# Kernel optimization log

Measured on AMD Instinct MI355X. Metric: run time of the kernel, lower is better.

## Reference

```python
import jax, jax.numpy as jnp
import numpy as np

B, S, IN, H, NH, PF, L = 8, 1024, 256, 1024, 16, 4096, 6
HD = H // NH
EPS = 1e-5


def _layernorm(x, g, b):
    m = jnp.mean(x, axis=-1, keepdims=True)
    v = jnp.mean((x - m) ** 2, axis=-1, keepdims=True)
    return (x - m) * jax.lax.rsqrt(v + EPS) * g + b


def setup_inputs() -> dict:
    key = jax.random.key(0)
    ks = iter(jax.random.split(key, 40))
    sd = 0.02
    inp = {
        "input_x": jax.random.normal(next(ks), (B, S, IN), jnp.float32),
        "emb_W": jax.random.normal(next(ks), (IN, H), jnp.float32) * sd,
        "emb_b": jnp.zeros((H,), jnp.float32),
        "pos_tab": jax.random.normal(next(ks), (S, H), jnp.float32) * sd,
        "Wq": jax.random.normal(next(ks), (L, H, H), jnp.float32) * sd,
        "bq": jnp.zeros((L, H), jnp.float32),
        "Wk": jax.random.normal(next(ks), (L, H, H), jnp.float32) * sd,
        "bk": jnp.zeros((L, H), jnp.float32),
        "Wv": jax.random.normal(next(ks), (L, H, H), jnp.float32) * sd,
        "bv": jnp.zeros((L, H), jnp.float32),
        "Wo": jax.random.normal(next(ks), (L, H, H), jnp.float32) * sd,
        "bo": jnp.zeros((L, H), jnp.float32),
        "ln1_g": jnp.ones((L, H), jnp.float32),
        "ln1_b": jnp.zeros((L, H), jnp.float32),
        "W1": jax.random.normal(next(ks), (L, H, PF), jnp.float32) * sd,
        "b1": jnp.zeros((L, PF), jnp.float32),
        "W2": jax.random.normal(next(ks), (L, PF, H), jnp.float32) * sd,
        "b2": jnp.zeros((L, H), jnp.float32),
        "ln2_g": jnp.ones((L, H), jnp.float32),
        "ln2_b": jnp.zeros((L, H), jnp.float32),
    }
    return inp


def _encoder(input_x, emb_W, emb_b, pos_tab, Wq, bq, Wk, bk, Wv, bv, Wo, bo,
             ln1_g, ln1_b, W1, b1, W2, b2, ln2_g, ln2_b):
    scale = jnp.sqrt(jnp.float32(H))  # module scales by sqrt(hidden_size)
    x = (input_x @ emb_W + emb_b) * scale + pos_tab[None, :, :]  # [B,S,H]

    def layer(x, p):
        wq, bq_, wk, bk_, wv, bv_, wo, bo_, g1, be1, w1, b1_, w2, b2_, g2, be2 = p
        q = (x @ wq + bq_).reshape(B, S, NH, HD).transpose(0, 2, 1, 3)  # bhsd
        k = (x @ wk + bk_).reshape(B, S, NH, HD).transpose(0, 2, 1, 3)
        v = (x @ wv + bv_).reshape(B, S, NH, HD).transpose(0, 2, 1, 3)
        energy = jnp.einsum("bhqd,bhkd->bhqk", q, k) / scale  # NOTE: /sqrt(H)
        attn = jax.nn.softmax(energy, axis=-1)
        o = jnp.einsum("bhqk,bhkd->bhqd", attn, v)
        o = o.transpose(0, 2, 1, 3).reshape(B, S, H) @ wo + bo_
        x = _layernorm(x + o, g1, be1)
        f = jax.nn.relu(x @ w1 + b1_) @ w2 + b2_
        x = _layernorm(x + f, g2, be2)
        return x, None

    params = (Wq, bq, Wk, bk, Wv, bv, Wo, bo, ln1_g, ln1_b, W1, b1, W2, b2, ln2_g, ln2_b)
    x, _ = jax.lax.scan(layer, x, params)
    return x


def reference(input_x, emb_W, emb_b, pos_tab, Wq, bq, Wk, bk, Wv, bv, Wo, bo,
              ln1_g, ln1_b, W1, b1, W2, b2, ln2_g, ln2_b):
    return _encoder(input_x, emb_W, emb_b, pos_tab, Wq, bq, Wk, bk, Wv, bv,
                    Wo, bo, ln1_g, ln1_b, W1, b1, W2, b2, ln2_g, ln2_b)
```

## Files before the change

kernel.cpp:

```cpp
#include <hip/hip_runtime.h>

#define HDIM 1024
#define BB 8
#define SS 1024
#define NHEAD 16
#define PFF 4096
#define NLAYER 6
#define MM (BB*SS)

typedef __attribute__((ext_vector_type(8))) short bf16x8_t;
typedef __attribute__((ext_vector_type(4))) float f32x4_t;
typedef __attribute__((ext_vector_type(16))) float f32x16_t;

static __device__ __forceinline__ unsigned short f2b(float f) {
  unsigned int u = __float_as_uint(f);
  u += 0x7fffu + ((u >> 16) & 1u);
  return (unsigned short)(u >> 16);
}

static __device__ __forceinline__ unsigned pkbf(float lo, float hi) {
  unsigned r;
  asm("v_cvt_pk_bf16_f32 %0, %1, %2" : "=v"(r) : "v"(lo), "v"(hi));
  return r;
}

static __device__ __forceinline__ bf16x8_t mk8(unsigned a, unsigned b, unsigned c, unsigned d) {
  union { unsigned u[4]; bf16x8_t v; } x;
  x.u[0] = a; x.u[1] = b; x.u[2] = c; x.u[3] = d;
  return x.v;
}

static __device__ __forceinline__ void gload16(const void* g, void* l) {
  __builtin_amdgcn_global_load_lds((__attribute__((address_space(1))) void*)g,
                                   (__attribute__((address_space(3))) void*)l, 16, 0, 0);
}

__global__ __launch_bounds__(256) void cvt_bf16(const float* __restrict__ in,
                                                unsigned short* __restrict__ o, int n4) {
  const int i = blockIdx.x * 256 + threadIdx.x;
  if (i < n4) {
    const float4 v = ((const float4*)in)[i];
    ushort4 ob = { f2b(v.x), f2b(v.y), f2b(v.z), f2b(v.w) };
    ((ushort4*)o)[i] = ob;
  }
}

__global__ __launch_bounds__(256) void transpose_bf16(const float* __restrict__ in,
                                                      unsigned short* __restrict__ outT,
                                                      int R, int C) {
  __shared__ float tile[32][33];
  const int c0 = blockIdx.x * 32, r0 = blockIdx.y * 32;
  const int tx = threadIdx.x, ty = threadIdx.y;
#pragma unroll
  for (int i = 0; i < 4; ++i)
    tile[ty + 8*i][tx] = in[(size_t)(r0 + ty + 8*i) * C + c0 + tx];
  __syncthreads();
#pragma unroll
  for (int i = 0; i < 4; ++i)
    outT[(size_t)(c0 + ty + 8*i) * R + r0 + tx] = f2b(tile[tx][ty + 8*i]);
}

__global__ __launch_bounds__(256) void vtrans(const unsigned short* __restrict__ qkv,
                                              unsigned short* __restrict__ vt) {
  __shared__ unsigned short tile[32][34];
  const int s0 = blockIdx.x * 32;
  const int by = blockIdx.y;
  const int bh = by >> 1, dt = by & 1;
  const int b = bh >> 4, h = bh & 15;
  const int tx = threadIdx.x, ty = threadIdx.y;
  const unsigned short* src = qkv + ((size_t)(b * 1024 + s0)) * 3072 + 2048 + h * 64 + dt * 32;
#pragma unroll
  for (int i = 0; i < 4; ++i)
    tile[ty + 8*i][tx] = src[(size_t)(ty + 8*i) * 3072 + tx];
  __syncthreads();
  unsigned short* dst = vt + (size_t)(bh * 64 + dt * 32) * 1024 + s0;
#pragma unroll
  for (int i = 0; i < 4; ++i)
    dst[(size_t)(ty + 8*i) * 1024 + tx] = tile[tx][ty + 8*i];
}

__global__ __launch_bounds__(256) void concat_bias(const float* __restrict__ bq,
                                                   const float* __restrict__ bk,
                                                   const float* __restrict__ bv,
                                                   float* __restrict__ o) {
  const int i = blockIdx.x * 256 + threadIdx.x;
  o[i] = (i < 1024) ? bq[i] : ((i < 2048) ? bk[i - 1024] : bv[i - 2048]);
}

template<bool BIAS, bool RELU, bool RESID, bool EMB, bool WF32, bool WBF16>
__global__ __launch_bounds__(256) void gemm_bt(
    const unsigned short* __restrict__ A,
    const unsigned short* __restrict__ Bt,
    const float* __restrict__ bias,
    const float* __restrict__ resid,
    const float* __restrict__ pos,
    float* __restrict__ outf,
    unsigned short* __restrict__ outb,
    int M, int N, int K) {
  __shared__ __align__(1024) char smem[32768];
  const int t = threadIdx.x;
  const int lane = t & 63;
  const int w = t >> 6;
  const int wr = w >> 1, wc = w & 1;
  const int m0 = blockIdx.y * 128;
  const int n0 = blockIdx.x * 128;

  const f32x4_t z = {0.f, 0.f, 0.f, 0.f};
  f32x4_t acc[4][4];
#pragma unroll
  for (int i = 0; i < 4; ++i)
#pragma unroll
    for (int j = 0; j < 4; ++j) acc[i][j] = z;

  const int nkt = K >> 6;
  for (int kt = 0; kt < nkt; ++kt) {
#pragma unroll
    for (int i = 0; i < 4; ++i) {
      const int chunk = i * 4 + w;
      const int byteoff = chunk * 1024 + lane * 16;
      const int row = byteoff >> 7;
      const int scb = (byteoff & 127) ^ ((row & 7) << 4);
      gload16((const char*)A  + ((size_t)(m0 + row) * K + (kt << 6)) * 2 + scb,
              smem + chunk * 1024);
      gload16((const char*)Bt + ((size_t)(n0 + row) * K + (kt << 6)) * 2 + scb,
              smem + 16384 + chunk * 1024);
    }
    __syncthreads();
#pragma unroll
    for (int ks = 0; ks < 2; ++ks) {
      bf16x8_t af[4], bfv[4];
      const int cb = ks * 64 + ((lane >> 4) << 4);
#pragma unroll
      for (int i = 0; i < 4; ++i) {
        const int ra = wr * 64 + i * 16 + (lane & 15);
        af[i]  = *(const bf16x8_t*)(smem + ra * 128 + (cb ^ ((ra & 7) << 4)));
        const int rb = wc * 64 + i * 16 + (lane & 15);
        bfv[i] = *(const bf16x8_t*)(smem + 16384 + rb * 128 + (cb ^ ((rb & 7) << 4)));
      }
#pragma unroll
      for (int i = 0; i < 4; ++i)
#pragma unroll
        for (int j = 0; j < 4; ++j)
          acc[i][j] = __builtin_amdgcn_mfma_f32_16x16x32_bf16(af[i], bfv[j], acc[i][j], 0, 0, 0);
    }
    __syncthreads();
  }

#pragma unroll
  for (int i = 0; i < 4; ++i) {
    const int rbase = m0 + wr * 64 + i * 16 + ((lane >> 4) << 2);
#pragma unroll
    for (int j = 0; j < 4; ++j) {
      const int cc = n0 + wc * 64 + j * 16 + (lane & 15);
      float bv = 0.f;
      if (BIAS) bv = bias[cc];
#pragma unroll
      for (int r = 0; r < 4; ++r) {
        const int row = rbase + r;
        float v = acc[i][j][r] + bv;
        if (EMB)  v = v * 32.f + pos[(size_t)(row & (SS - 1)) * N + cc];
        if (RELU) v = fmaxf(v, 0.f);
        if (RESID) v += resid[(size_t)row * N + cc];
        if (WF32)  outf[(size_t)row * N + cc] = v;
        if (WBF16) outb[(size_t)row * N + cc] = f2b(v);
      }
    }
  }
}

__global__ __launch_bounds__(256) void attn2(
    const unsigned short* __restrict__ qkv,
    const unsigned short* __restrict__ vt,
    unsigned short* __restrict__ O) {
  __shared__ __align__(1024) char smem[2 * 16384];
  const int t = threadIdx.x, lane = t & 63, w = t >> 6;
  const int l31 = lane & 31, lg = lane >> 5;
  const int bh = blockIdx.y;
  const int b = bh >> 4, h = bh & 15;
  const size_t rowb = (size_t)b << 10;
  const int q0 = blockIdx.x * 128 + w * 32;

  bf16x8_t qf[4];
  {
    const unsigned short* Qp = qkv + (rowb + q0 + l31) * 3072 + h * 64 + lg * 8;
#pragma unroll
    for (int dd = 0; dd < 4; ++dd) qf[dd] = *(const bf16x8_t*)(Qp + dd * 16);
  }

  f32x16_t oa0, oa1;
#pragma unroll
  for (int r = 0; r < 16; ++r) { oa0[r] = 0.f; oa1[r] = 0.f; }
  float m_run = -1e30f, l_run = 0.f;
  const float inv32 = 1.f / 32.f;

  const char* kglob = (const char*)qkv + ((size_t)1024 + h * 64) * 2;
  const char* vglob = (const char*)vt + (size_t)bh * 64 * 1024 * 2;

  auto stage = [&](int kt, int buf) {
    char* kbuf = smem + buf * 16384;
    char* vbuf = kbuf + 8192;
#pragma unroll
    for (int i = 0; i < 2; ++i) {
      const int chunk = w * 2 + i;
      const int byteoff = chunk * 1024 + lane * 16;
      const int row = byteoff >> 7;
      const int scb = (byteoff & 127) ^ ((row & 7) << 4);
      gload16(kglob + (size_t)(rowb + kt * 64 + row) * 6144 + scb, kbuf + chunk * 1024);
      gload16(vglob + ((size_t)row * 1024 + kt * 64) * 2 + scb,    vbuf + chunk * 1024);
    }
  };

  stage(0, 0);
  for (int kt = 0; kt < 16; ++kt) {
    const int cb = kt & 1;
    __syncthreads();
    if (kt < 15) stage(kt + 1, cb ^ 1);
    const char* kbuf = smem + cb * 16384;
    const char* vbuf = kbuf + 8192;

    f32x16_t p0, p1;
#pragma unroll
    for (int r = 0; r < 16; ++r) { p0[r] = 0.f; p1[r] = 0.f; }
    __builtin_amdgcn_s_setprio(1);
#pragma unroll
    for (int dd = 0; dd < 4; ++dd) {
      {
        const int row = l31;
        const int col = (dd * 32 + (lg << 4)) ^ ((row & 7) << 4);
        bf16x8_t kf = *(const bf16x8_t*)(kbuf + row * 128 + col);
        p0 = __builtin_amdgcn_mfma_f32_32x32x16_bf16(kf, qf[dd], p0, 0, 0, 0);
      }
      {
        const int row = 32 + l31;
        const int col = (dd * 32 + (lg << 4)) ^ ((row & 7) << 4);
        bf16x8_t kf = *(const bf16x8_t*)(kbuf + row * 128 + col);
        p1 = __builtin_amdgcn_mfma_f32_32x32x16_bf16(kf, qf[dd], p1, 0, 0, 0);
      }
    }
    __builtin_amdgcn_s_setprio(0);

    float mx = p0[0];
#pragma unroll
    for (int r = 1; r < 16; ++r) mx = fmaxf(mx, p0[r]);
#pragma unroll
    for (int r = 0; r < 16; ++r) mx = fmaxf(mx, p1[r]);
    mx = fmaxf(mx, __shfl_xor(mx, 32));
    const float mn = fmaxf(m_run, mx * inv32);
    const float fr = __expf(m_run - mn);
    m_run = mn;
    float sum = 0.f;
#pragma unroll
    for (int r = 0; r < 16; ++r) { const float e = __expf(p0[r] * inv32 - mn); p0[r] = e; sum += e; }
#pragma unroll
    for (int r = 0; r < 16; ++r) { const float e = __expf(p1[r] * inv32 - mn); p1[r] = e; sum += e; }
    sum += __shfl_xor(sum, 32);
    l_run = l_run * fr + sum;
#pragma unroll
    for (int r = 0; r < 16; ++r) { oa0[r] *= fr; oa1[r] *= fr; }

    const unsigned A0 = pkbf(p0[0], p0[1]),  B0 = pkbf(p0[2], p0[3]);
    const unsigned C0 = pkbf(p0[4], p0[5]),  D0 = pkbf(p0[6], p0[7]);
    const unsigned E0 = pkbf(p0[8], p0[9]),  F0 = pkbf(p0[10], p0[11]);
    const unsigned G0 = pkbf(p0[12], p0[13]), H0 = pkbf(p0[14], p0[15]);
    const unsigned A1 = pkbf(p1[0], p1[1]),  B1 = pkbf(p1[2], p1[3]);
    const unsigned C1 = pkbf(p1[4], p1[5]),  D1 = pkbf(p1[6], p1[7]);
    const unsigned E1 = pkbf(p1[8], p1[9]),  F1 = pkbf(p1[10], p1[11]);
    const unsigned G1 = pkbf(p1[12], p1[13]), H1 = pkbf(p1[14], p1[15]);
    const unsigned sA0 = __shfl_xor((int)A0, 32), sB0 = __shfl_xor((int)B0, 32);
    const unsigned sC0 = __shfl_xor((int)C0, 32), sD0 = __shfl_xor((int)D0, 32);
    const unsigned sE0 = __shfl_xor((int)E0, 32), sF0 = __shfl_xor((int)F0, 32);
    const unsigned sG0 = __shfl_xor((int)G0, 32), sH0 = __shfl_xor((int)H0, 32);
    const unsigned sA1 = __shfl_xor((int)A1, 32), sB1 = __shfl_xor((int)B1, 32);
    const unsigned sC1 = __shfl_xor((int)C1, 32), sD1 = __shfl_xor((int)D1, 32);
    const unsigned sE1 = __shfl_xor((int)E1, 32), sF1 = __shfl_xor((int)F1, 32);
    const unsigned sG1 = __shfl_xor((int)G1, 32), sH1 = __shfl_xor((int)H1, 32);
    const bool hi = (lg != 0);
    bf16x8_t pf[4];
    pf[0] = hi ? mk8(sC0, sD0, C0, D0) : mk8(A0, B0, sA0, sB0);
    pf[1] = hi ? mk8(sG0, sH0, G0, H0) : mk8(E0, F0, sE0, sF0);
    pf[2] = hi ? mk8(sC1, sD1, C1, D1) : mk8(A1, B1, sA1, sB1);
    pf[3] = hi ? mk8(sG1, sH1, G1, H1) : mk8(E1, F1, sE1, sF1);

    __builtin_amdgcn_s_setprio(1);
#pragma unroll
    for (int c = 0; c < 4; ++c) {
      {
        const int row = l31;
        const int col = (c * 32 + (lg << 4)) ^ ((row & 7) << 4);
        bf16x8_t vf = *(const bf16x8_t*)(vbuf + row * 128 + col);
        oa0 = __builtin_amdgcn_mfma_f32_32x32x16_bf16(vf, pf[c], oa0, 0, 0, 0);
      }
      {
        const int row = 32 + l31;
        const int col = (c * 32 + (lg << 4)) ^ ((row & 7) << 4);
        bf16x8_t vf = *(const bf16x8_t*)(vbuf + row * 128 + col);
        oa1 = __builtin_amdgcn_mfma_f32_32x32x16_bf16(vf, pf[c], oa1, 0, 0, 0);
      }
    }
    __builtin_amdgcn_s_setprio(0);
  }

  const float inv = 1.f / l_run;
  unsigned short* op = O + (rowb + q0 + l31) * 1024 + h * 64 + (lg << 2);
#pragma unroll
  for (int rg = 0; rg < 4; ++rg) {
    const unsigned u0 = pkbf(oa0[rg * 4 + 0] * inv, oa0[rg * 4 + 1] * inv);
    const unsigned u1 = pkbf(oa0[rg * 4 + 2] * inv, oa0[rg * 4 + 3] * inv);
    uint2 st = { u0, u1 };
    *(uint2*)(op + rg * 8) = st;
    const unsigned v0 = pkbf(oa1[rg * 4 + 0] * inv, oa1[rg * 4 + 1] * inv);
    const unsigned v1 = pkbf(oa1[rg * 4 + 2] * inv, oa1[rg * 4 + 3] * inv);
    uint2 st2 = { v0, v1 };
    *(uint2*)(op + 32 + rg * 8) = st2;
  }
}

__global__ __launch_bounds__(256) void ln_kernel(
    const float* __restrict__ y, const float* __restrict__ g, const float* __restrict__ be,
    float* __restrict__ xf, unsigned short* __restrict__ xb) {
  const int row = blockIdx.x;
  const int t = threadIdx.x;
  const float4 v = ((const float4*)(y + (size_t)row * HDIM))[t];
  float s  = v.x + v.y + v.z + v.w;
  float ss = v.x*v.x + v.y*v.y + v.z*v.z + v.w*v.w;
#pragma unroll
  for (int m = 1; m < 64; m <<= 1) { s += __shfl_xor(s, m); ss += __shfl_xor(ss, m); }
  __shared__ float rs[4], rss[4];
  const int w = t >> 6, lane = t & 63;
  if (lane == 0) { rs[w] = s; rss[w] = ss; }
  __syncthreads();
  s  = rs[0] + rs[1] + rs[2] + rs[3];
  ss = rss[0] + rss[1] + rss[2] + rss[3];
  const float mean = s * (1.f / HDIM);
  const float inv = rsqrtf(ss * (1.f / HDIM) - mean * mean + 1e-5f);
  const int c = t * 4;
  const float4 gg = *(const float4*)(g + c);
  const float4 bb = *(const float4*)(be + c);
  float4 o;
  o.x = (v.x - mean) * inv * gg.x + bb.x;
  o.y = (v.y - mean) * inv * gg.y + bb.y;
  o.z = (v.z - mean) * inv * gg.z + bb.z;
  o.w = (v.w - mean) * inv * gg.w + bb.w;
  ((float4*)(xf + (size_t)row * HDIM))[t] = o;
  ushort4 ob = { f2b(o.x), f2b(o.y), f2b(o.z), f2b(o.w) };
  ((ushort4*)(xb + (size_t)row * HDIM))[t] = ob;
}

extern "C" void kernel_launch(void* const* d_in, const int* in_sizes, int n_in,
                              void* d_out, int out_size, void* d_ws, size_t ws_size,
                              hipStream_t stream) {
  const float* input_x = (const float*)d_in[0];
  const float* emb_W   = (const float*)d_in[1];
  const float* emb_b   = (const float*)d_in[2];
  const float* pos_tab = (const float*)d_in[3];
  const float* Wq  = (const float*)d_in[4];
  const float* bq  = (const float*)d_in[5];
  const float* Wk  = (const float*)d_in[6];
  const float* bk  = (const float*)d_in[7];
  const float* Wv  = (const float*)d_in[8];
  const float* bv  = (const float*)d_in[9];
  const float* Wo  = (const float*)d_in[10];
  const float* bo  = (const float*)d_in[11];
  const float* ln1g = (const float*)d_in[12];
  const float* ln1b = (const float*)d_in[13];
  const float* W1  = (const float*)d_in[14];
  const float* b1  = (const float*)d_in[15];
  const float* W2  = (const float*)d_in[16];
  const float* b2  = (const float*)d_in[17];
  const float* ln2g = (const float*)d_in[18];
  const float* ln2b = (const float*)d_in[19];
  float* out = (float*)d_out;

  char* ws = (char*)d_ws;
  size_t off = 0;
  auto alloc = [&](size_t bytes) {
    char* p = ws + off;
    off += (bytes + 255) & ~(size_t)255;
    return p;
  };
  unsigned short* wqkvT = (unsigned short*)alloc((size_t)3072 * HDIM * 2);
  unsigned short* woT   = (unsigned short*)alloc((size_t)HDIM * HDIM * 2);
  unsigned short* w1T   = (unsigned short*)alloc((size_t)PFF * HDIM * 2);
  unsigned short* w2T   = (unsigned short*)alloc((size_t)HDIM * PFF * 2);
  unsigned short* embWT = (unsigned short*)alloc((size_t)HDIM * 256 * 2);
  float*          bqkv  = (float*)alloc(3072 * 4);
  unsigned short* inb   = (unsigned short*)alloc((size_t)MM * 256 * 2);
  unsigned short* xb    = (unsigned short*)alloc((size_t)MM * HDIM * 2);
  unsigned short* qkvb  = (unsigned short*)alloc((size_t)MM * 3072 * 2);
  unsigned short* vtb   = (unsigned short*)alloc((size_t)MM * HDIM * 2);
  unsigned short* ab    = (unsigned short*)alloc((size_t)MM * HDIM * 2);
  float* y = (float*)alloc((size_t)MM * HDIM * 4);
  unsigned short* hb = qkvb;

  const dim3 blk256(256);
  const dim3 tblk(32, 8);

  cvt_bf16<<<dim3(MM * 256 / 4 / 256), blk256, 0, stream>>>(input_x, inb, MM * 256 / 4);
  transpose_bf16<<<dim3(HDIM / 32, 256 / 32), tblk, 0, stream>>>(emb_W, embWT, 256, HDIM);

  gemm_bt<true, false, false, true, true, true><<<dim3(HDIM / 128, MM / 128), blk256, 0, stream>>>(
      inb, embWT, emb_b, nullptr, pos_tab, out, xb, MM, HDIM, 256);

  for (int l = 0; l < NLAYER; ++l) {
    const size_t wofs = (size_t)l * HDIM * HDIM;
    transpose_bf16<<<dim3(32, 32), tblk, 0, stream>>>(Wq + wofs, wqkvT,                 HDIM, HDIM);
    transpose_bf16<<<dim3(32, 32), tblk, 0, stream>>>(Wk + wofs, wqkvT + 1024 * 1024,   HDIM, HDIM);
    transpose_bf16<<<dim3(32, 32), tblk, 0, stream>>>(Wv + wofs, wqkvT + 2048 * 1024,   HDIM, HDIM);
    transpose_bf16<<<dim3(32, 32), tblk, 0, stream>>>(Wo + wofs, woT, HDIM, HDIM);
    transpose_bf16<<<dim3(PFF / 32, HDIM / 32), tblk, 0, stream>>>(
        W1 + (size_t)l * HDIM * PFF, w1T, HDIM, PFF);
    transpose_bf16<<<dim3(HDIM / 32, PFF / 32), tblk, 0, stream>>>(
        W2 + (size_t)l * PFF * HDIM, w2T, PFF, HDIM);
    concat_bias<<<dim3(12), blk256, 0, stream>>>(bq + l * HDIM, bk + l * HDIM, bv + l * HDIM, bqkv);

    gemm_bt<true, false, false, false, false, true><<<dim3(24, 64), blk256, 0, stream>>>(
        xb, wqkvT, bqkv, nullptr, nullptr, nullptr, qkvb, MM, 3072, HDIM);

    vtrans<<<dim3(32, 256), tblk, 0, stream>>>(qkvb, vtb);

    attn2<<<dim3(SS / 128, BB * NHEAD), blk256, 0, stream>>>(qkvb, vtb, ab);

    gemm_bt<true, false, true, false, true, false><<<dim3(8, 64), blk256, 0, stream>>>(
        ab, woT, bo + l * HDIM, out, nullptr, y, nullptr, MM, HDIM, HDIM);
    ln_kernel<<<dim3(MM), blk256, 0, stream>>>(y, ln1g + l * HDIM, ln1b + l * HDIM, out, xb);

    gemm_bt<true, true, false, false, false, true><<<dim3(PFF / 128, MM / 128), blk256, 0, stream>>>(
        xb, w1T, b1 + (size_t)l * PFF, nullptr, nullptr, nullptr, hb, MM, PFF, HDIM);
    gemm_bt<true, false, true, false, true, false><<<dim3(8, 64), blk256, 0, stream>>>(
        hb, w2T, b2 + l * HDIM, out, nullptr, y, nullptr, MM, HDIM, PFF);
    ln_kernel<<<dim3(MM), blk256, 0, stream>>>(y, ln2g + l * HDIM, ln2b + l * HDIM, out, xb);
  }
  (void)in_sizes; (void)n_in; (void)out_size; (void)ws_size;
}
```

Baseline: 2.470 ms.

## Replace GEMM with 256-row double-buffered tiles, 8 waves, and XCD-aware block remap

The 128x128, 4-wave GEMM is replaced by a 512-thread kernel that computes 256xBN tiles (BN 128 or 256 per call site). LDS is double-buffered with global_load_lds prefetch of the next K-tile, paced by explicit vmcnt waits and raw barriers. Block IDs are remapped across the 8 XCDs to improve L2 locality, and s_setprio raises priority around the MFMA bursts. The goal is to hide global load latency and raise arithmetic intensity per block. In exchange it uses far more registers and LDS (up to 128KB for BN=256), and with launch_bounds(512,2) that could cap occupancy or cause spills.

```diff
diff --git a/kernel.cpp b/kernel.cpp
--- a/kernel.cpp
+++ b/kernel.cpp
@@ -33,6 +33,17 @@
 static __device__ __forceinline__ void gload16(const void* g, void* l) {
   __builtin_amdgcn_global_load_lds((__attribute__((address_space(1))) void*)g,
                                    (__attribute__((address_space(3))) void*)l, 16, 0, 0);
+}
+
+template<int N>
+static __device__ __forceinline__ void vwait() {
+  asm volatile("s_waitcnt vmcnt(%0)" :: "n"(N) : "memory");
+}
+
+static __device__ __forceinline__ void bar() {
+  asm volatile("" ::: "memory");
+  __builtin_amdgcn_s_barrier();
+  asm volatile("" ::: "memory");
 }
 
 __global__ __launch_bounds__(256) void cvt_bf16(const float* __restrict__ in,
@@ -87,8 +98,8 @@
   o[i] = (i < 1024) ? bq[i] : ((i < 2048) ? bk[i - 1024] : bv[i - 2048]);
 }
 
-template<bool BIAS, bool RELU, bool RESID, bool EMB, bool WF32, bool WBF16>
-__global__ __launch_bounds__(256) void gemm_bt(
+template<int BN, bool BIAS, bool RELU, bool RESID, bool EMB, bool WF32, bool WBF16>
+__global__ __launch_bounds__(512, 2) void gemm256(
     const unsigned short* __restrict__ A,
     const unsigned short* __restrict__ Bt,
     const float* __restrict__ bias,
@@ -97,61 +108,125 @@
     float* __restrict__ outf,
     unsigned short* __restrict__ outb,
     int M, int N, int K) {
-  __shared__ __align__(1024) char smem[32768];
-  const int t = threadIdx.x;
-  const int lane = t & 63;
-  const int w = t >> 6;
-  const int wr = w >> 1, wc = w & 1;
-  const int m0 = blockIdx.y * 128;
-  const int n0 = blockIdx.x * 128;
+  constexpr int BUFSZ = 32768 + BN * 128;
+  constexpr int NJ = BN / 64;
+  constexpr int WCN = BN / 4;
+  constexpr int BI = BN / 64;
+  constexpr int LPT = 4 + BI;
+  __shared__ __align__(1024) char smem[2 * BUFSZ];
+  const int t = threadIdx.x, lane = t & 63, w = t >> 6;
+  const int wr = w >> 2, wc = w & 3;
+
+  int flat = blockIdx.x + gridDim.x * blockIdx.y;
+  const int cpx = (gridDim.x * gridDim.y) >> 3;
+  flat = (flat & 7) * cpx + (flat >> 3);
+  const int m0 = (flat / gridDim.x) * 256;
+  const int n0 = (flat % gridDim.x) * BN;
 
   const f32x4_t z = {0.f, 0.f, 0.f, 0.f};
-  f32x4_t acc[4][4];
-#pragma unroll
-  for (int i = 0; i < 4; ++i)
-#pragma unroll
-    for (int j = 0; j < 4; ++j) acc[i][j] = z;
-
-  const int nkt = K >> 6;
-  for (int kt = 0; kt < nkt; ++kt) {
+  f32x4_t acc[8][NJ];
+#pragma unroll
+  for (int i = 0; i < 8; ++i)
+#pragma unroll
+    for (int j = 0; j < NJ; ++j) acc[i][j] = z;
+
+  auto stage = [&](int kt, int buf) {
+    char* ab_ = smem + buf * BUFSZ;
+    char* bb_ = ab_ + 32768;
 #pragma unroll
     for (int i = 0; i < 4; ++i) {
-      const int chunk = i * 4 + w;
+      const int chunk = i * 8 + w;
       const int byteoff = chunk * 1024 + lane * 16;
       const int row = byteoff >> 7;
       const int scb = (byteoff & 127) ^ ((row & 7) << 4);
-      gload16((const char*)A  + ((size_t)(m0 + row) * K + (kt << 6)) * 2 + scb,
-              smem + chunk * 1024);
+      gload16((const char*)A + ((size_t)(m0 + row) * K + (kt << 6)) * 2 + scb,
+              ab_ + chunk * 1024);
+    }
+#pragma unroll
+    for (int i = 0; i < BI; ++i) {
+      const int chunk = i * 8 + w;
+      const int byteoff = chunk * 1024 + lane * 16;
+      const int row = byteoff >> 7;
+      const int scb = (byteoff & 127) ^ ((row & 7) << 4);
       gload16((const char*)Bt + ((size_t)(n0 + row) * K + (kt << 6)) * 2 + scb,
-              smem + 16384 + chunk * 1024);
-    }
-    __syncthreads();
-#pragma unroll
-    for (int ks = 0; ks < 2; ++ks) {
-      bf16x8_t af[4], bfv[4];
-      const int cb = ks * 64 + ((lane >> 4) << 4);
-#pragma unroll
-      for (int i = 0; i < 4; ++i) {
-        const int ra = wr * 64 + i * 16 + (lane & 15);
-        af[i]  = *(const bf16x8_t*)(smem + ra * 128 + (cb ^ ((ra & 7) << 4)));
-        const int rb = wc * 64 + i * 16 + (lane & 15);
-        bfv[i] = *(const bf16x8_t*)(smem + 16384 + rb * 128 + (cb ^ ((rb & 7) << 4)));
-      }
+              bb_ + chunk * 1024);
+    }
+  };
+
+  const int nkt = K >> 6;
+  stage(0, 0);
+  stage(1, 1);
+  vwait<LPT>();
+  bar();
+
+  int cur = 0;
+  for (int kt = 0; kt < nkt; ++kt) {
+    const char* ab_ = smem + cur * BUFSZ;
+    const char* bb_ = ab_ + 32768;
+
+    bf16x8_t bfr[NJ][2], afr[4][2];
+#pragma unroll
+    for (int j = 0; j < NJ; ++j)
+#pragma unroll
+      for (int ks = 0; ks < 2; ++ks) {
+        const int row = wc * WCN + j * 16 + (lane & 15);
+        const int cb = ks * 64 + ((lane >> 4) << 4);
+        bfr[j][ks] = *(const bf16x8_t*)(bb_ + row * 128 + (cb ^ ((row & 7) << 4)));
+      }
+#pragma unroll
+    for (int i = 0; i < 4; ++i)
+#pragma unroll
+      for (int ks = 0; ks < 2; ++ks) {
+        const int row = wr * 128 + i * 16 + (lane & 15);
+        const int cb = ks * 64 + ((lane >> 4) << 4);
+        afr[i][ks] = *(const bf16x8_t*)(ab_ + row * 128 + (cb ^ ((row & 7) << 4)));
+      }
+    __builtin_amdgcn_s_setprio(1);
+#pragma unroll
+    for (int ks = 0; ks < 2; ++ks)
 #pragma unroll
       for (int i = 0; i < 4; ++i)
 #pragma unroll
-        for (int j = 0; j < 4; ++j)
-          acc[i][j] = __builtin_amdgcn_mfma_f32_16x16x32_bf16(af[i], bfv[j], acc[i][j], 0, 0, 0);
-    }
-    __syncthreads();
-  }
-
-#pragma unroll
-  for (int i = 0; i < 4; ++i) {
-    const int rbase = m0 + wr * 64 + i * 16 + ((lane >> 4) << 2);
-#pragma unroll
-    for (int j = 0; j < 4; ++j) {
-      const int cc = n0 + wc * 64 + j * 16 + (lane & 15);
+        for (int j = 0; j < NJ; ++j)
+          acc[i][j] = __builtin_amdgcn_mfma_f32_16x16x32_bf16(afr[i][ks], bfr[j][ks], acc[i][j], 0, 0, 0);
+    __builtin_amdgcn_s_setprio(0);
+#pragma unroll
+    for (int i = 0; i < 4; ++i)
+#pragma unroll
+      for (int ks = 0; ks < 2; ++ks) {
+        const int row = wr * 128 + 64 + i * 16 + (lane & 15);
+        const int cb = ks * 64 + ((lane >> 4) << 4);
+        afr[i][ks] = *(const bf16x8_t*)(ab_ + row * 128 + (cb ^ ((row & 7) << 4)));
+      }
+    __builtin_amdgcn_s_setprio(1);
+#pragma unroll
+    for (int ks = 0; ks < 2; ++ks)
+#pragma unroll
+      for (int i = 0; i < 4; ++i)
+#pragma unroll
+        for (int j = 0; j < NJ; ++j)
+          acc[4 + i][j] = __builtin_amdgcn_mfma_f32_16x16x32_bf16(afr[i][ks], bfr[j][ks], acc[4 + i][j], 0, 0, 0);
+    __builtin_amdgcn_s_setprio(0);
+
+    if (kt + 1 < nkt) {
+      bar();
+      if (kt + 2 < nkt) {
+        stage(kt + 2, cur);
+        vwait<LPT>();
+      } else {
+        vwait<0>();
+      }
+      bar();
+    }
+    cur ^= 1;
+  }
+
+#pragma unroll
+  for (int i = 0; i < 8; ++i) {
+    const int rbase = m0 + wr * 128 + i * 16 + ((lane >> 4) << 2);
+#pragma unroll
+    for (int j = 0; j < NJ; ++j) {
+      const int cc = n0 + wc * WCN + j * 16 + (lane & 15);
       float bv = 0.f;
       if (BIAS) bv = bias[cc];
 #pragma unroll
@@ -393,19 +468,20 @@
   unsigned short* hb = qkvb;
 
   const dim3 blk256(256);
+  const dim3 blk512(512);
   const dim3 tblk(32, 8);
 
   cvt_bf16<<<dim3(MM * 256 / 4 / 256), blk256, 0, stream>>>(input_x, inb, MM * 256 / 4);
   transpose_bf16<<<dim3(HDIM / 32, 256 / 32), tblk, 0, stream>>>(emb_W, embWT, 256, HDIM);
 
-  gemm_bt<true, false, false, true, true, true><<<dim3(HDIM / 128, MM / 128), blk256, 0, stream>>>(
+  gemm256<128, true, false, false, true, true, true><<<dim3(HDIM / 128, MM / 256), blk512, 0, stream>>>(
       inb, embWT, emb_b, nullptr, pos_tab, out, xb, MM, HDIM, 256);
 
   for (int l = 0; l < NLAYER; ++l) {
     const size_t wofs = (size_t)l * HDIM * HDIM;
-    transpose_bf16<<<dim3(32, 32), tblk, 0, stream>>>(Wq + wofs, wqkvT,                 HDIM, HDIM);
-    transpose_bf16<<<dim3(32, 32), tblk, 0, stream>>>(Wk + wofs, wqkvT + 1024 * 1024,   HDIM, HDIM);
-    transpose_bf16<<<dim3(32, 32), tblk, 0, stream>>>(Wv + wofs, wqkvT + 2048 * 1024,   HDIM, HDIM);
+    transpose_bf16<<<dim3(32, 32), tblk, 0, stream>>>(Wq + wofs, wqkvT,               HDIM, HDIM);
+    transpose_bf16<<<dim3(32, 32), tblk, 0, stream>>>(Wk + wofs, wqkvT + 1024 * 1024, HDIM, HDIM);
+    transpose_bf16<<<dim3(32, 32), tblk, 0, stream>>>(Wv + wofs, wqkvT + 2048 * 1024, HDIM, HDIM);
     transpose_bf16<<<dim3(32, 32), tblk, 0, stream>>>(Wo + wofs, woT, HDIM, HDIM);
     transpose_bf16<<<dim3(PFF / 32, HDIM / 32), tblk, 0, stream>>>(
         W1 + (size_t)l * HDIM * PFF, w1T, HDIM, PFF);
@@ -413,20 +489,20 @@
         W2 + (size_t)l * PFF * HDIM, w2T, PFF, HDIM);
     concat_bias<<<dim3(12), blk256, 0, stream>>>(bq + l * HDIM, bk + l * HDIM, bv + l * HDIM, bqkv);
 
-    gemm_bt<true, false, false, false, false, true><<<dim3(24, 64), blk256, 0, stream>>>(
+    gemm256<256, true, false, false, false, false, true><<<dim3(3072 / 256, MM / 256), blk512, 0, stream>>>(
         xb, wqkvT, bqkv, nullptr, nullptr, nullptr, qkvb, MM, 3072, HDIM);
 
     vtrans<<<dim3(32, 256), tblk, 0, stream>>>(qkvb, vtb);
 
     attn2<<<dim3(SS / 128, BB * NHEAD), blk256, 0, stream>>>(qkvb, vtb, ab);
 
-    gemm_bt<true, false, true, false, true, false><<<dim3(8, 64), blk256, 0, stream>>>(
+    gemm256<128, true, false, true, false, true, false><<<dim3(HDIM / 128, MM / 256), blk512, 0, stream>>>(
         ab, woT, bo + l * HDIM, out, nullptr, y, nullptr, MM, HDIM, HDIM);
     ln_kernel<<<dim3(MM), blk256, 0, stream>>>(y, ln1g + l * HDIM, ln1b + l * HDIM, out, xb);
 
-    gemm_bt<true, true, false, false, false, true><<<dim3(PFF / 128, MM / 128), blk256, 0, stream>>>(
+    gemm256<256, true, true, false, false, false, true><<<dim3(PFF / 256, MM / 256), blk512, 0, stream>>>(
         xb, w1T, b1 + (size_t)l * PFF, nullptr, nullptr, nullptr, hb, MM, PFF, HDIM);
-    gemm_bt<true, false, true, false, true, false><<<dim3(8, 64), blk256, 0, stream>>>(
+    gemm256<128, true, false, true, false, true, false><<<dim3(HDIM / 128, MM / 256), blk512, 0, stream>>>(
         hb, w2T, b2 + l * HDIM, out, nullptr, y, nullptr, MM, HDIM, PFF);
     ln_kernel<<<dim3(MM), blk256, 0, stream>>>(y, ln2g + l * HDIM, ln2b + l * HDIM, out, xb);
   }
```

Result: faster. 2.280 ms (-7.7%).
